# Performance work log

Hardware: AMD Instinct MI355X
Metric: run time of the kernel (lower is better)

Reference implementation:

```python
import jax, jax.numpy as jnp
import numpy as np

K, D = 512, 256
NUM_CLASSES, SHARED_KEYS = 10, 10
B, H, W = 32, 64, 64
TRAINING = True


def setup_inputs() -> dict:
    key = jax.random.key(0)
    k1, k2, k3 = jax.random.split(key, 3)
    z_e_x = jax.random.normal(k1, (B, D, H, W), dtype=jnp.float32)
    labels = jax.random.randint(k2, (B,), 0, NUM_CLASSES)
    # nn.Embedding weight initialized uniform(-1/K, 1/K)
    codebook = jax.random.uniform(k3, (K, D), minval=-1.0 / K, maxval=1.0 / K,
                                  dtype=jnp.float32)
    return {"z_e_x": z_e_x, "codebook": codebook, "labels": labels}


def _irrelevant_regions(labels_flat, k, num_classes, n_shared, training):
    # uniform partition of the first K - n_shared codes over the classes
    uniform = jnp.round(jnp.linspace(-0.5, num_classes - 0.51, k - n_shared))  # [K-Ns]
    irrel = uniform[None, :] != labels_flat[:, None].astype(uniform.dtype)     # [N, K-Ns]
    n = labels_flat.shape[0]
    if training:
        tail = jnp.ones((n, n_shared), dtype=bool)   # TRAIN: shared keys masked out
    else:
        tail = jnp.zeros((n, n_shared), dtype=bool)
    return jnp.concatenate([irrel, tail], axis=1)    # [N, K]


def reference(z_e_x, codebook, labels):
    x = jnp.transpose(z_e_x, (0, 2, 3, 1))           # [B,H,W,D]
    xf = x.reshape(-1, D)                            # [N,D], N=B*H*W
    labels_flat = jnp.repeat(labels, H * W)          # [N]

    irrel = _irrelevant_regions(labels_flat, K, NUM_CLASSES, SHARED_KEYS, TRAINING)

    cb_sqr = jnp.sum(codebook * codebook, axis=1)                      # [K]
    in_sqr = jnp.sum(xf * xf, axis=1, keepdims=True)                   # [N,1]
    distances = in_sqr + cb_sqr[None, :] - 2.0 * (xf @ codebook.T)     # [N,K]
    distances = jnp.where(irrel, jnp.inf, distances)

    idx = jnp.argmin(distances, axis=1)                                # [N]

    codes = codebook[idx].reshape(x.shape)                             # [B,H,W,D]
    # straight-through path (detached codebook in torch)
    z_q = x + jax.lax.stop_gradient(codes - x)
    z_q_x = jnp.transpose(z_q, (0, 3, 1, 2))                           # [B,D,H,W]
    # non-detached codebook lookup path
    z_q_bar = codebook[jax.lax.stop_gradient(idx)].reshape(x.shape)
    z_q_x_bar = jnp.transpose(z_q_bar, (0, 3, 1, 2))                   # [B,D,H,W]
    return (z_q_x, z_q_x_bar)
```

## Files before the change

kernel.cpp:

```cpp
#include <hip/hip_runtime.h>


#define D       256
#define KCODES  512
#define HW      4096
#define BATCH   32
#define NPTS    (BATCH * HW)
#define MAXC    51

__constant__ int c_cls_start[11] = {0, 51, 101, 151, 201, 251, 301, 352, 402, 452, 502};

__global__ __launch_bounds__(256) void prep_kernel(const float* __restrict__ cb,
                                                   float* __restrict__ cbT,
                                                   float* __restrict__ cbs) {
    const int k = blockIdx.x;
    const int d = threadIdx.x;
    float v = cb[k * D + d];
    cbT[(size_t)d * KCODES + k] = v;
    __shared__ double red[256];
    red[d] = (double)v * (double)v;
    __syncthreads();
    for (int s = 128; s > 0; s >>= 1) {
        if (d < s) red[d] += red[d + s];
        __syncthreads();
    }
    if (d == 0) cbs[k] = (float)red[0];
}

__global__ __launch_bounds__(256) void vq_kernel(const float* __restrict__ z,
                                                 const int* __restrict__ labels,
                                                 const float* __restrict__ cbT,
                                                 const float* __restrict__ cbs,
                                                 float* __restrict__ out) {
    const int b   = blockIdx.x >> 4;
    const int hw  = ((blockIdx.x & 15) << 8) | threadIdx.x;
    const int lab = __builtin_amdgcn_readfirstlane(labels[b]);
    const int c0  = c_cls_start[lab];
    const int cnt = c_cls_start[lab + 1] - c0;

    const float* __restrict__ xp = z + (size_t)b * (D * HW) + hw;

    float acc[MAXC];
#pragma unroll
    for (int k = 0; k < MAXC; ++k) acc[k] = 0.0f;

    double xsq = 0.0;

    float xb[4];
#pragma unroll
    for (int i = 0; i < 4; ++i) xb[i] = xp[(size_t)i * HW];

    for (int d = 0; d < D; d += 4) {
        float xn[4];
#pragma unroll
        for (int i = 0; i < 4; ++i) {
            int dn = (d + 4 + i) & (D - 1);
            xn[i] = xp[(size_t)dn * HW];
        }
#pragma unroll
        for (int i = 0; i < 4; ++i) {
            const float* __restrict__ wd = cbT + (size_t)(d + i) * KCODES + c0;
            const float x = xb[i];
            xsq = fma((double)x, (double)x, xsq);
#pragma unroll
            for (int k = 0; k < MAXC; ++k)
                acc[k] = fmaf(x, wd[k], acc[k]);
        }
#pragma unroll
        for (int i = 0; i < 4; ++i) xb[i] = xn[i];
    }

    const float insq = (float)xsq;
    float best = __builtin_inff();
    int i1 = c0;
#pragma unroll
    for (int k = 0; k < MAXC; ++k) {
        if (k < cnt) {
            float T    = insq + cbs[c0 + k];
            float dist = fmaf(-2.0f, acc[k], T);
            if (dist < best) { best = dist; i1 = c0 + k; }
        }
    }

    float* __restrict__ o0 = out + (size_t)b * (D * HW) + hw;
    float* __restrict__ o1 = o0 + (size_t)NPTS * D;
    const int ci = i1;
    for (int d = 0; d < D; ++d) {
        float v = cbT[(size_t)d * KCODES + ci];
        o0[(size_t)d * HW] = v;
        o1[(size_t)d * HW] = v;
    }
}

extern "C" void kernel_launch(void* const* d_in, const int* in_sizes, int n_in,
                              void* d_out, int out_size, void* d_ws, size_t ws_size,
                              hipStream_t stream) {
    const float* z      = (const float*)d_in[0];
    const float* cb     = (const float*)d_in[1];
    const int*   labels = (const int*)d_in[2];
    float* out = (float*)d_out;

    float* cbT = (float*)d_ws;
    float* cbs = cbT + (size_t)D * KCODES;

    hipLaunchKernelGGL(prep_kernel, dim3(KCODES), dim3(D), 0, stream, cb, cbT, cbs);
    hipLaunchKernelGGL(vq_kernel, dim3(NPTS / 256), dim3(256), 0, stream,
                       z, labels, cbT, cbs, out);
}
```

Measured before the change: 447.3 us.

## Split codebook search across waves and reduce argmin via shared memory

Each block now handles 64 points, and its four waves each evaluate a 13-code slice of the label's codebook range. Partial argmins are combined through shared memory. The output gather is then split so each wave writes a quarter of the D channels. This cuts per-thread register pressure and launches four times more blocks to raise occupancy and latency hiding. In exchange, each input point is read by four waves, which adds redundant loads of z and a block barrier.

```diff
diff --git a/kernel.cpp b/kernel.cpp
--- a/kernel.cpp
+++ b/kernel.cpp
@@ -6,7 +6,7 @@
 #define HW      4096
 #define BATCH   32
 #define NPTS    (BATCH * HW)
-#define MAXC    51
+#define WPW     13
 
 __constant__ int c_cls_start[11] = {0, 51, 101, 151, 201, 251, 301, 352, 402, 452, 502};
 
@@ -32,17 +32,21 @@
                                                  const float* __restrict__ cbT,
                                                  const float* __restrict__ cbs,
                                                  float* __restrict__ out) {
-    const int b   = blockIdx.x >> 4;
-    const int hw  = ((blockIdx.x & 15) << 8) | threadIdx.x;
-    const int lab = __builtin_amdgcn_readfirstlane(labels[b]);
-    const int c0  = c_cls_start[lab];
-    const int cnt = c_cls_start[lab + 1] - c0;
+    const int lane = threadIdx.x & 63;
+    const int w    = __builtin_amdgcn_readfirstlane(threadIdx.x >> 6);
+    const int b    = blockIdx.x >> 6;
+    const int hw   = ((blockIdx.x & 63) << 6) | lane;
+    const int lab  = __builtin_amdgcn_readfirstlane(labels[b]);
+    const int c0   = c_cls_start[lab];
+    const int cnt  = c_cls_start[lab + 1] - c0;
+    const int kbase = c0 + w * WPW;
+    const int myn   = min(WPW, cnt - w * WPW);
 
     const float* __restrict__ xp = z + (size_t)b * (D * HW) + hw;
 
-    float acc[MAXC];
+    float acc[WPW];
 #pragma unroll
-    for (int k = 0; k < MAXC; ++k) acc[k] = 0.0f;
+    for (int j = 0; j < WPW; ++j) acc[j] = 0.0f;
 
     double xsq = 0.0;
 
@@ -59,12 +63,12 @@
         }
 #pragma unroll
         for (int i = 0; i < 4; ++i) {
-            const float* __restrict__ wd = cbT + (size_t)(d + i) * KCODES + c0;
+            const float* __restrict__ wd = cbT + (size_t)(d + i) * KCODES + kbase;
             const float x = xb[i];
             xsq = fma((double)x, (double)x, xsq);
 #pragma unroll
-            for (int k = 0; k < MAXC; ++k)
-                acc[k] = fmaf(x, wd[k], acc[k]);
+            for (int j = 0; j < WPW; ++j)
+                acc[j] = fmaf(x, wd[j], acc[j]);
         }
 #pragma unroll
         for (int i = 0; i < 4; ++i) xb[i] = xn[i];
@@ -72,21 +76,34 @@
 
     const float insq = (float)xsq;
     float best = __builtin_inff();
-    int i1 = c0;
+    int bi = kbase;
 #pragma unroll
-    for (int k = 0; k < MAXC; ++k) {
-        if (k < cnt) {
-            float T    = insq + cbs[c0 + k];
-            float dist = fmaf(-2.0f, acc[k], T);
-            if (dist < best) { best = dist; i1 = c0 + k; }
+    for (int j = 0; j < WPW; ++j) {
+        if (j < myn) {
+            float T    = insq + cbs[kbase + j];
+            float dist = fmaf(-2.0f, acc[j], T);
+            if (dist < best) { best = dist; bi = kbase + j; }
         }
+    }
+
+    __shared__ float sd[4][64];
+    __shared__ int   si[4][64];
+    sd[w][lane] = best;
+    si[w][lane] = bi;
+    __syncthreads();
+    float fb = sd[0][lane];
+    int   fi = si[0][lane];
+#pragma unroll
+    for (int w2 = 1; w2 < 4; ++w2) {
+        float dv = sd[w2][lane];
+        if (dv < fb) { fb = dv; fi = si[w2][lane]; }
     }
 
     float* __restrict__ o0 = out + (size_t)b * (D * HW) + hw;
     float* __restrict__ o1 = o0 + (size_t)NPTS * D;
-    const int ci = i1;
-    for (int d = 0; d < D; ++d) {
-        float v = cbT[(size_t)d * KCODES + ci];
+    const int d0 = w * 64;
+    for (int d = d0; d < d0 + 64; ++d) {
+        float v = cbT[(size_t)d * KCODES + fi];
         o0[(size_t)d * HW] = v;
         o1[(size_t)d * HW] = v;
     }
@@ -104,6 +121,6 @@
     float* cbs = cbT + (size_t)D * KCODES;
 
     hipLaunchKernelGGL(prep_kernel, dim3(KCODES), dim3(D), 0, stream, cb, cbT, cbs);
-    hipLaunchKernelGGL(vq_kernel, dim3(NPTS / 256), dim3(256), 0, stream,
+    hipLaunchKernelGGL(vq_kernel, dim3(NPTS / 64), dim3(256), 0, stream,
                        z, labels, cbT, cbs, out);
 }
```

After: 404.2 us. -9.6%, faster.
